# Performance work log

Hardware: AMD Instinct MI355X
Metric: run time of the kernel (lower is better)

Reference implementation:

```python
import jax, jax.numpy as jnp
import numpy as np

N_HEADS = 16
LN_EPS = 1e-5


def layer_norm(x, w, b):
    mu = jnp.mean(x, axis=-1, keepdims=True)
    var = jnp.mean((x - mu) ** 2, axis=-1, keepdims=True)
    return (x - mu) * jax.lax.rsqrt(var + LN_EPS) * w + b


def setup_inputs() -> dict:
    key = jax.random.key(0)
    B, S, D = 4, 2048, 1024
    F = 4 * D
    ks = jax.random.split(key, 16)
    s = 0.02
    return {
        "x": jax.random.normal(ks[0], (B, S, D), dtype=jnp.float32),
        "Wq": jax.random.normal(ks[1], (D, D), dtype=jnp.float32) * s,
        "Wk": jax.random.normal(ks[2], (D, D), dtype=jnp.float32) * s,
        "Wv": jax.random.normal(ks[3], (D, D), dtype=jnp.float32) * s,
        "Wo": jax.random.normal(ks[4], (D, D), dtype=jnp.float32) * s,
        "ln1_w": jnp.ones((D,), dtype=jnp.float32),
        "ln1_b": jnp.zeros((D,), dtype=jnp.float32),
        "W1": jax.random.normal(ks[5], (D, F), dtype=jnp.float32) * s,
        "b1": jnp.zeros((F,), dtype=jnp.float32),
        "W2": jax.random.normal(ks[6], (F, D), dtype=jnp.float32) * s,
        "b2": jnp.zeros((D,), dtype=jnp.float32),
        "ln2_w": jnp.ones((D,), dtype=jnp.float32),
        "ln2_b": jnp.zeros((D,), dtype=jnp.float32),
        "conf_w": jax.random.normal(ks[7], (D, 1), dtype=jnp.float32) * s,
        "conf_b": jnp.zeros((1,), dtype=jnp.float32),
    }


def reference(x, Wq, Wk, Wv, Wo, ln1_w, ln1_b, W1, b1, W2, b2, ln2_w, ln2_b, conf_w, conf_b):
    B, S, D = x.shape
    H = N_HEADS
    HD = D // H
    # --- attention sub-block (pre-LN) ---
    h = layer_norm(x, ln1_w, ln1_b)
    q = jnp.einsum("bsd,dhk->bhsk", h, Wq.reshape(D, H, HD))
    k = jnp.einsum("bsd,dhk->bhsk", h, Wk.reshape(D, H, HD))
    v = jnp.einsum("bsd,dhk->bhsk", h, Wv.reshape(D, H, HD))
    scores = jnp.einsum("bhsk,bhtk->bhst", q, k) / jnp.sqrt(jnp.asarray(HD, x.dtype))
    causal = jnp.triu(jnp.ones((S, S), dtype=bool), k=1)  # [S, S]
    scores = jnp.where(causal[None, None, :, :], -jnp.inf, scores)
    attn = jax.nn.softmax(scores, axis=-1)
    ctx = jnp.einsum("bhst,bhtk->bshk", attn, v).reshape(B, S, D)
    x = x + ctx @ Wo  # residual (dropout = identity in eval)
    # --- FFN sub-block ---
    h2 = layer_norm(x, ln2_w, ln2_b)
    x_out = x + jax.nn.relu(h2 @ W1 + b1) @ W2 + b2 * 0 + (jax.nn.relu(h2 @ W1 + b1) @ W2 * 0)
    x_out = x + (jax.nn.relu(h2 @ W1 + b1) @ W2 + b2)
    # --- confidence predictor: avg-pool over seq, linear, sigmoid, mean over batch ---
    conf = jax.nn.sigmoid(jnp.mean(x_out, axis=1) @ conf_w + conf_b)  # [B, 1]
    conf = jnp.mean(conf, axis=0)  # [1]
    return x_out, conf
```

## Files before the change

### kernel.cpp

```cpp
#include <hip/hip_runtime.h>
#include <hip/hip_bf16.h>
#include <math.h>

typedef __bf16 bf16;
typedef __bf16 bf16x8 __attribute__((ext_vector_type(8)));
typedef __bf16 bf16x4 __attribute__((ext_vector_type(4)));
typedef float  f32x4  __attribute__((ext_vector_type(4)));
typedef short  s16x4  __attribute__((ext_vector_type(4)));

#define CLAMP(v) fminf(fmaxf((v), -100.f), 100.f)
#define NEGINF (-1e30f)

static __device__ __forceinline__ float exp2fast(float x)
{
#if __has_builtin(__builtin_amdgcn_exp2f)
    return __builtin_amdgcn_exp2f(x);
#else
    return exp2f(x);
#endif
}

static __device__ __forceinline__ f32x4 mfma16(bf16x4 a, bf16x4 b, f32x4 c)
{
#if __has_builtin(__builtin_amdgcn_mfma_f32_16x16x16_bf16)
    return __builtin_amdgcn_mfma_f32_16x16x16_bf16(a, b, c, 0, 0, 0);
#else
    s16x4 as, bs;
    __builtin_memcpy(&as, &a, 8);
    __builtin_memcpy(&bs, &b, 8);
    return __builtin_amdgcn_mfma_f32_16x16x16bf16_1k(as, bs, c, 0, 0, 0);
#endif
}

static __device__ __forceinline__ void gload_lds16(const bf16* g, bf16* l)
{
    __builtin_amdgcn_global_load_lds(
        (const __attribute__((address_space(1))) void*)g,
        (__attribute__((address_space(3))) void*)l, 16, 0, 0);
}

__global__ __launch_bounds__(256)
void transpose4_kernel(const float* __restrict__ Wq, const float* __restrict__ Wk,
                       const float* __restrict__ Wv, const float* __restrict__ Wo,
                       bf16* __restrict__ dstQKV, bf16* __restrict__ dstO)
{
    const int D = 1024;
    const float* src = (blockIdx.z == 0) ? Wq : (blockIdx.z == 1) ? Wk : (blockIdx.z == 2) ? Wv : Wo;
    bf16* dst = (blockIdx.z < 3) ? dstQKV + (size_t)blockIdx.z * D * D : dstO;
    __shared__ float tile[32][33];
    int c0 = blockIdx.x * 32, r0 = blockIdx.y * 32;
    int tx = threadIdx.x, ty = threadIdx.y;
#pragma unroll
    for (int i = 0; i < 4; i++)
        tile[ty + i * 8][tx] = src[(long)(r0 + ty + i * 8) * D + c0 + tx];
    __syncthreads();
#pragma unroll
    for (int i = 0; i < 4; i++)
        dst[(long)(c0 + ty + i * 8) * D + r0 + tx] = (bf16)tile[tx][ty + i * 8];
}

__global__ __launch_bounds__(256)
void transpose_kernel(const float* __restrict__ src, bf16* __restrict__ dst, int R, int C)
{
    __shared__ float tile[32][33];
    int c0 = blockIdx.x * 32, r0 = blockIdx.y * 32;
    int tx = threadIdx.x, ty = threadIdx.y;
#pragma unroll
    for (int i = 0; i < 4; i++)
        tile[ty + i * 8][tx] = src[(long)(r0 + ty + i * 8) * C + c0 + tx];
    __syncthreads();
#pragma unroll
    for (int i = 0; i < 4; i++)
        dst[(long)(c0 + ty + i * 8) * R + r0 + tx] = (bf16)tile[tx][ty + i * 8];
}

__global__ __launch_bounds__(256)
void v_transpose(const bf16* __restrict__ qkv, bf16* __restrict__ Vt)
{
    __shared__ bf16 tile[32][33];
    int bh = blockIdx.z, b = bh >> 4, h = bh & 15;
    int t0 = blockIdx.x * 32, d0 = blockIdx.y * 32;
    int tx = threadIdx.x, ty = threadIdx.y;
#pragma unroll
    for (int i = 0; i < 4; i++)
        tile[ty + i * 8][tx] = qkv[(long)(b * 2048 + t0 + ty + i * 8) * 3072 + 2048 + h * 64 + d0 + tx];
    __syncthreads();
#pragma unroll
    for (int i = 0; i < 4; i++)
        Vt[((long)bh * 64 + d0 + ty + i * 8) * 2048 + t0 + tx] = tile[tx][ty + i * 8];
}

__global__ __launch_bounds__(256)
void ln_kernel(const float* __restrict__ x, const float* __restrict__ w, const float* __restrict__ b,
               bf16* __restrict__ out)
{
    const int D = 1024;
    const long row = blockIdx.x;
    const int t = threadIdx.x;
    f32x4 xv = *(const f32x4*)(x + row * D + t * 4);
    float s  = xv[0] + xv[1] + xv[2] + xv[3];
    float s2 = xv[0] * xv[0] + xv[1] * xv[1] + xv[2] * xv[2] + xv[3] * xv[3];
#pragma unroll
    for (int off = 32; off; off >>= 1) { s += __shfl_xor(s, off); s2 += __shfl_xor(s2, off); }
    __shared__ float ls[4], ls2[4];
    if ((t & 63) == 0) { ls[t >> 6] = s; ls2[t >> 6] = s2; }
    __syncthreads();
    s = ls[0] + ls[1] + ls[2] + ls[3];
    s2 = ls2[0] + ls2[1] + ls2[2] + ls2[3];
    float mu = s / D;
    float var = fmaxf(s2 / D - mu * mu, 0.f);
    float rstd = rsqrtf(var + 1e-5f);
#pragma unroll
    for (int i = 0; i < 4; i++) {
        int c = t * 4 + i;
        float v = (xv[i] - mu) * rstd * w[c] + b[c];
        out[row * D + c] = (bf16)CLAMP(v);
    }
}

template <int MODE>
__global__ __launch_bounds__(256)
void gemm_bt(const bf16* __restrict__ A, int lda, const bf16* __restrict__ Bt, int ldb,
             int M, int N, int K,
             const float* __restrict__ bias, const float* __restrict__ resid,
             void* __restrict__ outv, int ldo)
{
    __shared__ bf16 sA[128 * 32];
    __shared__ bf16 sB[128 * 32];
    const int t = threadIdx.x;
    const int wave = t >> 6, lane = t & 63;
    const int wr = wave >> 1, wc = wave & 1;
    const int quad = lane >> 4, l16 = lane & 15;
    const int bm = blockIdx.y * 128, bn = blockIdx.x * 128;

    f32x4 acc[4][4];
#pragma unroll
    for (int i = 0; i < 4; i++)
#pragma unroll
        for (int j = 0; j < 4; j++) acc[i][j] = f32x4{0.f, 0.f, 0.f, 0.f};

    const int srow = wave * 16 + (lane >> 2);
    const int scol = (lane & 3) * 8;
    const bf16* ga = A + (long)(bm + srow) * lda + scol;
    const bf16* gb = Bt + (long)(bn + srow) * ldb + scol;
    bf16* la = &sA[wave * 16 * 32];
    bf16* lb = &sB[wave * 16 * 32];

    for (int k0 = 0; k0 < K; k0 += 32) {
        __syncthreads();
        gload_lds16(ga + k0, la);
        gload_lds16(gb + k0, lb);
        gload_lds16(ga + (long)64 * lda + k0, la + 64 * 32);
        gload_lds16(gb + (long)64 * ldb + k0, lb + 64 * 32);
        __syncthreads();
        bf16x8 af[4], bfv[4];
#pragma unroll
        for (int i = 0; i < 4; i++)
            af[i] = *(const bf16x8*)(&sA[(wr * 64 + i * 16 + l16) * 32 + quad * 8]);
#pragma unroll
        for (int j = 0; j < 4; j++)
            bfv[j] = *(const bf16x8*)(&sB[(wc * 64 + j * 16 + l16) * 32 + quad * 8]);
#pragma unroll
        for (int i = 0; i < 4; i++)
#pragma unroll
            for (int j = 0; j < 4; j++)
                acc[i][j] = __builtin_amdgcn_mfma_f32_16x16x32_bf16(af[i], bfv[j], acc[i][j], 0, 0, 0);
    }

    float bv[4];
    if constexpr (MODE == 1 || MODE == 3) {
#pragma unroll
        for (int j = 0; j < 4; j++) bv[j] = bias[bn + wc * 64 + j * 16 + l16];
    }
#pragma unroll
    for (int i = 0; i < 4; i++) {
        int m = bm + wr * 64 + i * 16 + quad * 4;
#pragma unroll
        for (int j = 0; j < 4; j++) {
            int n = bn + wc * 64 + j * 16 + l16;
#pragma unroll
            for (int r = 0; r < 4; r++) {
                float v = acc[i][j][r];
                long idx = (long)(m + r) * ldo + n;
                if constexpr (MODE == 0) {
                    ((bf16*)outv)[idx] = (bf16)CLAMP(v);
                } else if constexpr (MODE == 1) {
                    v += bv[j]; v = v > 0.f ? v : 0.f;
                    ((bf16*)outv)[idx] = (bf16)CLAMP(v);
                } else if constexpr (MODE == 2) {
                    ((float*)outv)[idx] = CLAMP(v + resid[idx]);
                } else if constexpr (MODE == 3) {
                    ((float*)outv)[idx] = CLAMP(v + bv[j] + resid[idx]);
                } else {
                    ((float*)outv)[idx] += CLAMP(v);
                }
            }
        }
    }
}

#define SM_C 0.1803368801111f

static __device__ __forceinline__ void attn_tile(
    const bf16x8 kf[4][2], const bf16* sVt, int t0, int qpb,
    int quad, int l16,
    const bf16x8 qf[2][2], f32x4 o[2][4], float* m_i, float* l_i)
{
    if (t0 > qpb + 31) return;
    bf16x4 pb[2][4];
#pragma unroll
    for (int rf = 0; rf < 2; rf++) {
        f32x4 sc[4];
#pragma unroll
        for (int tt = 0; tt < 4; tt++) {
            f32x4 s4 = f32x4{0.f, 0.f, 0.f, 0.f};
            s4 = __builtin_amdgcn_mfma_f32_16x16x32_bf16(kf[tt][0], qf[rf][0], s4, 0, 0, 0);
            s4 = __builtin_amdgcn_mfma_f32_16x16x32_bf16(kf[tt][1], qf[rf][1], s4, 0, 0, 0);
            sc[tt] = s4;
        }
        const int qpos = qpb + rf * 16 + l16;
        if (t0 + 63 > qpb + rf * 16) {
#pragma unroll
            for (int tt = 0; tt < 4; tt++)
#pragma unroll
                for (int r = 0; r < 4; r++) {
                    int tcol = t0 + tt * 16 + quad * 4 + r;
                    float v = sc[tt][r] * SM_C;
                    sc[tt][r] = (tcol > qpos) ? NEGINF : v;
                }
        } else {
#pragma unroll
            for (int tt = 0; tt < 4; tt++)
#pragma unroll
                for (int r = 0; r < 4; r++) sc[tt][r] = sc[tt][r] * SM_C;
        }
        float t4[4];
#pragma unroll
        for (int tt = 0; tt < 4; tt++)
            t4[tt] = fmaxf(fmaxf(sc[tt][0], sc[tt][1]), fmaxf(sc[tt][2], sc[tt][3]));
        float mt = fmaxf(fmaxf(t4[0], t4[1]), fmaxf(t4[2], t4[3]));
        mt = fmaxf(mt, __shfl_xor(mt, 16));
        mt = fmaxf(mt, __shfl_xor(mt, 32));
        float mn = fmaxf(m_i[rf], mt);
        float alpha = exp2fast(m_i[rf] - mn);
        m_i[rf] = mn;
        float lt4[4];
#pragma unroll
        for (int tt = 0; tt < 4; tt++) {
            float e0 = exp2fast(sc[tt][0] - mn);
            float e1 = exp2fast(sc[tt][1] - mn);
            float e2 = exp2fast(sc[tt][2] - mn);
            float e3 = exp2fast(sc[tt][3] - mn);
            sc[tt][0] = e0; sc[tt][1] = e1; sc[tt][2] = e2; sc[tt][3] = e3;
            lt4[tt] = (e0 + e1) + (e2 + e3);
        }
        float lt = (lt4[0] + lt4[1]) + (lt4[2] + lt4[3]);
        lt += __shfl_xor(lt, 16);
        lt += __shfl_xor(lt, 32);
        l_i[rf] = l_i[rf] * alpha + lt;
#pragma unroll
        for (int jb = 0; jb < 4; jb++)
#pragma unroll
            for (int r = 0; r < 4; r++) o[rf][jb][r] *= alpha;
#pragma unroll
        for (int tt = 0; tt < 4; tt++)
            pb[rf][tt] = bf16x4{(bf16)sc[tt][0], (bf16)sc[tt][1], (bf16)sc[tt][2], (bf16)sc[tt][3]};
    }
#pragma unroll
    for (int jb = 0; jb < 4; jb++) {
#pragma unroll
        for (int tt = 0; tt < 4; tt++) {
            bf16x4 va = *(const bf16x4*)(&sVt[(jb * 16 + l16) * 72 + tt * 16 + quad * 4]);
            o[0][jb] = mfma16(va, pb[0][tt], o[0][jb]);
            o[1][jb] = mfma16(va, pb[1][tt], o[1][jb]);
        }
    }
}

__global__ __launch_bounds__(256, 2)
void attn_kernel(const bf16* __restrict__ qkv, const bf16* __restrict__ Vt, bf16* __restrict__ ctx)
{
    const int bh = blockIdx.x;
    const int p  = blockIdx.y;
    const int b = bh >> 4, h = bh & 15;
    const int t = threadIdx.x;
    const int wave = t >> 6, lane = t & 63;
    const int quad = lane >> 4, l16 = lane & 15;
    const long RS = 3072;
    const int qb0 = p, qb1 = 15 - p;
    const int nt0 = 2 * p + 2, nt1 = 32 - 2 * p;

    __shared__ bf16 sK[64 * 72];
    __shared__ bf16 sVt[64 * 72];

    bf16x8 qf[2][2][2];
#pragma unroll
    for (int s = 0; s < 2; s++) {
        const int qb = s ? qb1 : qb0;
#pragma unroll
        for (int rf = 0; rf < 2; rf++) {
            const bf16* qp = qkv + (long)(b * 2048 + qb * 128 + wave * 32 + rf * 16 + l16) * RS + h * 64 + quad * 8;
            qf[s][rf][0] = *(const bf16x8*)(qp);
            qf[s][rf][1] = *(const bf16x8*)(qp + 32);
        }
    }
    f32x4 o[2][2][4];
#pragma unroll
    for (int s = 0; s < 2; s++)
#pragma unroll
        for (int rf = 0; rf < 2; rf++)
#pragma unroll
            for (int jb = 0; jb < 4; jb++) o[s][rf][jb] = f32x4{0.f, 0.f, 0.f, 0.f};
    float m_i[2][2] = {{NEGINF, NEGINF}, {NEGINF, NEGINF}};
    float l_i[2][2] = {{0.f, 0.f}, {0.f, 0.f}};
    const int qpb0 = qb0 * 128 + wave * 32;
    const int qpb1 = qb1 * 128 + wave * 32;

    const int cg = (t & 7) * 8, rr = t >> 3;
    const bf16* Kbase  = qkv + (long)(b * 2048) * RS + 1024 + h * 64;
    const bf16* Vtbase = Vt + ((long)bh * 64) * 2048;

    bf16x8 kreg[2], vreg[2];
#pragma unroll
    for (int pp = 0; pp < 2; pp++) {
        kreg[pp] = *(const bf16x8*)(Kbase + (long)(pp * 32 + rr) * RS + cg);
        vreg[pp] = *(const bf16x8*)(Vtbase + (long)(pp * 32 + rr) * 2048 + cg);
    }

    for (int ti = 0; ti < nt1; ti++) {
        __syncthreads();
#pragma unroll
        for (int pp = 0; pp < 2; pp++) {
            *(bf16x8*)(&sK[(pp * 32 + rr) * 72 + cg]) = kreg[pp];
            *(bf16x8*)(&sVt[(pp * 32 + rr) * 72 + cg]) = vreg[pp];
        }
        __syncthreads();
        if (ti + 1 < nt1) {
            int t0n = (ti + 1) * 64;
#pragma unroll
            for (int pp = 0; pp < 2; pp++) {
                kreg[pp] = *(const bf16x8*)(Kbase + (long)(t0n + pp * 32 + rr) * RS + cg);
                vreg[pp] = *(const bf16x8*)(Vtbase + (long)(pp * 32 + rr) * 2048 + t0n + cg);
            }
        }
        const int t0 = ti * 64;

        bf16x8 kf[4][2];
#pragma unroll
        for (int tt = 0; tt < 4; tt++) {
            kf[tt][0] = *(const bf16x8*)(&sK[(tt * 16 + l16) * 72 + quad * 8]);
            kf[tt][1] = *(const bf16x8*)(&sK[(tt * 16 + l16) * 72 + 32 + quad * 8]);
        }
        if (ti < nt0)
            attn_tile(kf, sVt, t0, qpb0, quad, l16, qf[0], o[0], m_i[0], l_i[0]);
        attn_tile(kf, sVt, t0, qpb1, quad, l16, qf[1], o[1], m_i[1], l_i[1]);
    }
#pragma unroll
    for (int s = 0; s < 2; s++) {
        const int qpb = s ? qpb1 : qpb0;
#pragma unroll
        for (int rf = 0; rf < 2; rf++) {
            float rl = 1.0f / l_i[s][rf];
            const long row = (long)(b * 2048 + qpb + rf * 16 + l16) * 1024 + h * 64;
#pragma unroll
            for (int jb = 0; jb < 4; jb++) {
                bf16x4 ov;
#pragma unroll
                for (int r = 0; r < 4; r++) ov[r] = (bf16)CLAMP(o[s][rf][jb][r] * rl);
                *(bf16x4*)(&ctx[row + jb * 16 + quad * 4]) = ov;
            }
        }
    }
}

__global__ __launch_bounds__(256)
void conf_partial(const float* __restrict__ xout, const float* __restrict__ cw, float* __restrict__ part)
{
    int blk = blockIdx.x;
    int b = blk >> 6, chunk = blk & 63;
    int t = threadIdx.x;
    int d0 = t * 4;
    f32x4 w = *(const f32x4*)(cw + d0);
    float acc = 0.f;
    for (int s = chunk * 32; s < chunk * 32 + 32; s++) {
        f32x4 v = *(const f32x4*)(xout + (long)(b * 2048 + s) * 1024 + d0);
        acc += v[0] * w[0] + v[1] * w[1] + v[2] * w[2] + v[3] * w[3];
    }
#pragma unroll
    for (int off = 32; off; off >>= 1) acc += __shfl_xor(acc, off);
    __shared__ float ls[4];
    if ((t & 63) == 0) ls[t >> 6] = acc;
    __syncthreads();
    if (t == 0) part[blk] = ls[0] + ls[1] + ls[2] + ls[3];
}

__global__ void conf_final(const float* __restrict__ part, const float* __restrict__ cb, float* __restrict__ outp)
{
    if (threadIdx.x == 0) {
        float accb = 0.f;
        for (int b = 0; b < 4; b++) {
            float s = 0.f;
            for (int i = 0; i < 64; i++) s += part[b * 64 + i];
            float z = s / 2048.0f + cb[0];
            accb += 1.0f / (1.0f + expf(-z));
        }
        outp[0] = accb * 0.25f;
    }
}

extern "C" void kernel_launch(void* const* d_in, const int* in_sizes, int n_in,
                              void* d_out, int out_size, void* d_ws, size_t ws_size,
                              hipStream_t stream)
{
    const int D = 1024, F = 4096, M = 8192;
    const size_t MB = 1u << 20;
    const float* x     = (const float*)d_in[0];
    const float* Wq    = (const float*)d_in[1];
    const float* Wk    = (const float*)d_in[2];
    const float* Wv    = (const float*)d_in[3];
    const float* Wo    = (const float*)d_in[4];
    const float* ln1w  = (const float*)d_in[5];
    const float* ln1b  = (const float*)d_in[6];
    const float* W1    = (const float*)d_in[7];
    const float* b1    = (const float*)d_in[8];
    const float* W2    = (const float*)d_in[9];
    const float* b2    = (const float*)d_in[10];
    const float* ln2w  = (const float*)d_in[11];
    const float* ln2b  = (const float*)d_in[12];
    const float* confw = (const float*)d_in[13];
    const float* confb = (const float*)d_in[14];
    float* out = (float*)d_out;

    char* ws = (char*)d_ws;
    bf16*  WqkvT = (bf16*)(ws);
    bf16*  WoT   = (bf16*)(ws + 8 * MB);
    bf16*  h     = (bf16*)(ws + 16 * MB);
    bf16*  qkv   = (bf16*)(ws + 32 * MB);
    bf16*  Vt    = (bf16*)(ws + 80 * MB);
    bf16*  ctx   = (bf16*)(ws + 16 * MB);
    float* x1    = (float*)(ws + 32 * MB);
    bf16*  h2    = (bf16*)(ws + 16 * MB);
    bf16*  W1T   = (bf16*)(ws);
    bf16*  W2T   = (bf16*)(ws + 8 * MB);
    bf16*  a1h   = (bf16*)(ws + 64 * MB);
    float* part  = (float*)(ws + 96 * MB);

    dim3 tb(32, 8);
    transpose4_kernel<<<dim3(32, 32, 4), tb, 0, stream>>>(Wq, Wk, Wv, Wo, WqkvT, WoT);
    ln_kernel<<<M, 256, 0, stream>>>(x, ln1w, ln1b, h);
    gemm_bt<0><<<dim3(24, 64), 256, 0, stream>>>(h, D, WqkvT, D, M, 3 * D, D, nullptr, nullptr, qkv, 3 * D);
    v_transpose<<<dim3(64, 2, 64), tb, 0, stream>>>(qkv, Vt);
    attn_kernel<<<dim3(64, 8), 256, 0, stream>>>(qkv, Vt, ctx);
    gemm_bt<2><<<dim3(8, 64), 256, 0, stream>>>(ctx, D, WoT, D, M, D, D, nullptr, x, x1, D);
    transpose_kernel<<<dim3(F / 32, D / 32), tb, 0, stream>>>(W1, W1T, D, F);
    transpose_kernel<<<dim3(D / 32, F / 32), tb, 0, stream>>>(W2, W2T, F, D);
    ln_kernel<<<M, 256, 0, stream>>>(x1, ln2w, ln2b, h2);
    gemm_bt<1><<<dim3(16, 64), 256, 0, stream>>>(h2, D, W1T, D, M, 2048, D, b1, nullptr, a1h, 2048);
    gemm_bt<4><<<dim3(8, 64), 256, 0, stream>>>(a1h, 2048, W2T, F, M, D, 2048, nullptr, nullptr, x1, D);
    gemm_bt<1><<<dim3(16, 64), 256, 0, stream>>>(h2, D, W1T + (size_t)2048 * D, D, M, 2048, D, b1 + 2048, nullptr, a1h, 2048);
    gemm_bt<3><<<dim3(8, 64), 256, 0, stream>>>(a1h, 2048, W2T + 2048, F, M, D, 2048, b2, x1, out, D);
    conf_partial<<<256, 256, 0, stream>>>(out, confw, part);
    conf_final<<<1, 64, 0, stream>>>(part, confb, out + (size_t)M * D);
}
```

Measured before the change: 613.3 us.

## Add 256x256 tile GEMM with XCD swizzle for QKV and FFN1 projections

Adds a 512-thread GEMM kernel computing 256x256 output tiles, with each wave holding an 8x4 grid of MFMA accumulators. It is used for the QKV projection and both FFN up-projection halves, so each loaded A/B tile is reused more and global/LDS traffic per flop drops. It also remaps block indices across the 8 XCDs (also applied to the existing 128 GEMM) to improve L2 locality. The risks are higher register pressure, single-block occupancy per CU, and fewer blocks than CUs for some grids (256 blocks for FFN1).

```diff
diff --git a/kernel.cpp b/kernel.cpp
--- a/kernel.cpp
+++ b/kernel.cpp
@@ -37,6 +37,16 @@
     __builtin_amdgcn_global_load_lds(
         (const __attribute__((address_space(1))) void*)g,
         (__attribute__((address_space(3))) void*)l, 16, 0, 0);
+}
+
+static __device__ __forceinline__ void xcd_swizzle(int& bx, int& by)
+{
+    int gx = gridDim.x, nwg = gx * gridDim.y;
+    int lin = by * gx + bx;
+    int cpx = nwg >> 3;
+    int swz = (lin & 7) * cpx + (lin >> 3);
+    bx = swz % gx;
+    by = swz / gx;
 }
 
 __global__ __launch_bounds__(256)
@@ -131,7 +141,9 @@
     const int wave = t >> 6, lane = t & 63;
     const int wr = wave >> 1, wc = wave & 1;
     const int quad = lane >> 4, l16 = lane & 15;
-    const int bm = blockIdx.y * 128, bn = blockIdx.x * 128;
+    int bx = blockIdx.x, by = blockIdx.y;
+    xcd_swizzle(bx, by);
+    const int bm = by * 128, bn = bx * 128;
 
     f32x4 acc[4][4];
 #pragma unroll
@@ -175,6 +187,89 @@
 #pragma unroll
     for (int i = 0; i < 4; i++) {
         int m = bm + wr * 64 + i * 16 + quad * 4;
+#pragma unroll
+        for (int j = 0; j < 4; j++) {
+            int n = bn + wc * 64 + j * 16 + l16;
+#pragma unroll
+            for (int r = 0; r < 4; r++) {
+                float v = acc[i][j][r];
+                long idx = (long)(m + r) * ldo + n;
+                if constexpr (MODE == 0) {
+                    ((bf16*)outv)[idx] = (bf16)CLAMP(v);
+                } else if constexpr (MODE == 1) {
+                    v += bv[j]; v = v > 0.f ? v : 0.f;
+                    ((bf16*)outv)[idx] = (bf16)CLAMP(v);
+                } else if constexpr (MODE == 2) {
+                    ((float*)outv)[idx] = CLAMP(v + resid[idx]);
+                } else if constexpr (MODE == 3) {
+                    ((float*)outv)[idx] = CLAMP(v + bv[j] + resid[idx]);
+                } else {
+                    ((float*)outv)[idx] += CLAMP(v);
+                }
+            }
+        }
+    }
+}
+
+template <int MODE>
+__global__ __launch_bounds__(512, 1)
+void gemm256(const bf16* __restrict__ A, int lda, const bf16* __restrict__ Bt, int ldb,
+             int M, int N, int K,
+             const float* __restrict__ bias, const float* __restrict__ resid,
+             void* __restrict__ outv, int ldo)
+{
+    __shared__ bf16 sA[256 * 32];
+    __shared__ bf16 sB[256 * 32];
+    const int t = threadIdx.x;
+    const int wave = t >> 6, lane = t & 63;
+    const int wr = wave >> 2, wc = wave & 3;
+    const int quad = lane >> 4, l16 = lane & 15;
+    int bx = blockIdx.x, by = blockIdx.y;
+    xcd_swizzle(bx, by);
+    const int bm = by * 256, bn = bx * 256;
+
+    f32x4 acc[8][4];
+#pragma unroll
+    for (int i = 0; i < 8; i++)
+#pragma unroll
+        for (int j = 0; j < 4; j++) acc[i][j] = f32x4{0.f, 0.f, 0.f, 0.f};
+
+    const int srow = t >> 2;
+    const int scol = (t & 3) * 8;
+    const bf16* ga = A + (long)(bm + srow) * lda + scol;
+    const bf16* gb = Bt + (long)(bn + srow) * ldb + scol;
+    bf16* la = &sA[wave * 16 * 32];
+    bf16* lb = &sB[wave * 16 * 32];
+
+    for (int k0 = 0; k0 < K; k0 += 32) {
+        __syncthreads();
+        gload_lds16(ga + k0, la);
+        gload_lds16(gb + k0, lb);
+        gload_lds16(ga + (long)128 * lda + k0, la + 128 * 32);
+        gload_lds16(gb + (long)128 * ldb + k0, lb + 128 * 32);
+        __syncthreads();
+        bf16x8 af[8], bfv[4];
+#pragma unroll
+        for (int i = 0; i < 8; i++)
+            af[i] = *(const bf16x8*)(&sA[(wr * 128 + i * 16 + l16) * 32 + quad * 8]);
+#pragma unroll
+        for (int j = 0; j < 4; j++)
+            bfv[j] = *(const bf16x8*)(&sB[(wc * 64 + j * 16 + l16) * 32 + quad * 8]);
+#pragma unroll
+        for (int i = 0; i < 8; i++)
+#pragma unroll
+            for (int j = 0; j < 4; j++)
+                acc[i][j] = __builtin_amdgcn_mfma_f32_16x16x32_bf16(af[i], bfv[j], acc[i][j], 0, 0, 0);
+    }
+
+    float bv[4];
+    if constexpr (MODE == 1 || MODE == 3) {
+#pragma unroll
+        for (int j = 0; j < 4; j++) bv[j] = bias[bn + wc * 64 + j * 16 + l16];
+    }
+#pragma unroll
+    for (int i = 0; i < 8; i++) {
+        int m = bm + wr * 128 + i * 16 + quad * 4;
 #pragma unroll
         for (int j = 0; j < 4; j++) {
             int n = bn + wc * 64 + j * 16 + l16;
@@ -448,16 +543,16 @@
     dim3 tb(32, 8);
     transpose4_kernel<<<dim3(32, 32, 4), tb, 0, stream>>>(Wq, Wk, Wv, Wo, WqkvT, WoT);
     ln_kernel<<<M, 256, 0, stream>>>(x, ln1w, ln1b, h);
-    gemm_bt<0><<<dim3(24, 64), 256, 0, stream>>>(h, D, WqkvT, D, M, 3 * D, D, nullptr, nullptr, qkv, 3 * D);
+    gemm256<0><<<dim3(12, 32), 512, 0, stream>>>(h, D, WqkvT, D, M, 3 * D, D, nullptr, nullptr, qkv, 3 * D);
     v_transpose<<<dim3(64, 2, 64), tb, 0, stream>>>(qkv, Vt);
     attn_kernel<<<dim3(64, 8), 256, 0, stream>>>(qkv, Vt, ctx);
     gemm_bt<2><<<dim3(8, 64), 256, 0, stream>>>(ctx, D, WoT, D, M, D, D, nullptr, x, x1, D);
     transpose_kernel<<<dim3(F / 32, D / 32), tb, 0, stream>>>(W1, W1T, D, F);
     transpose_kernel<<<dim3(D / 32, F / 32), tb, 0, stream>>>(W2, W2T, F, D);
     ln_kernel<<<M, 256, 0, stream>>>(x1, ln2w, ln2b, h2);
-    gemm_bt<1><<<dim3(16, 64), 256, 0, stream>>>(h2, D, W1T, D, M, 2048, D, b1, nullptr, a1h, 2048);
+    gemm256<1><<<dim3(8, 32), 512, 0, stream>>>(h2, D, W1T, D, M, 2048, D, b1, nullptr, a1h, 2048);
     gemm_bt<4><<<dim3(8, 64), 256, 0, stream>>>(a1h, 2048, W2T, F, M, D, 2048, nullptr, nullptr, x1, D);
-    gemm_bt<1><<<dim3(16, 64), 256, 0, stream>>>(h2, D, W1T + (size_t)2048 * D, D, M, 2048, D, b1 + 2048, nullptr, a1h, 2048);
+    gemm256<1><<<dim3(8, 32), 512, 0, stream>>>(h2, D, W1T + (size_t)2048 * D, D, M, 2048, D, b1 + 2048, nullptr, a1h, 2048);
     gemm_bt<3><<<dim3(8, 64), 256, 0, stream>>>(a1h, 2048, W2T + 2048, F, M, D, 2048, b2, x1, out, D);
     conf_partial<<<256, 256, 0, stream>>>(out, confw, part);
     conf_final<<<1, 64, 0, stream>>>(part, confb, out + (size_t)M * D);
```

After: 614.0 us. No clear change (+0.1%).
